# Performance work log

Hardware: AMD Instinct MI355X
Metric: run time of the kernel (lower is better)

The kernel has to match this reference:

```python
import jax, jax.numpy as jnp
import numpy as np

DT = 0.2   # dt
T = 30     # free-phase relaxation steps


def rho(x):
    return jnp.clip(x, 0.0, 1.0)


def rhop(x):
    return ((x >= 0.0) & (x <= 1.0)).astype(x.dtype)


def setup_inputs() -> dict:
    key = jax.random.key(0)
    ks = jax.random.split(key, 10)
    B = 2048
    L = [1024, 2048, 2048, 2048]  # fcLayers
    s0 = jax.random.uniform(ks[0], (B, L[0]), dtype=jnp.float32)
    s1 = jax.random.uniform(ks[1], (B, L[1]), dtype=jnp.float32)
    s2 = jax.random.uniform(ks[2], (B, L[2]), dtype=jnp.float32)
    data = jax.random.uniform(ks[3], (B, L[3]), dtype=jnp.float32)
    # W[i] = Linear(fcLayers[i+1], fcLayers[i]) -> weight [L[i], L[i+1]], fan_in = L[i+1]
    W0 = jax.random.normal(ks[4], (L[0], L[1]), dtype=jnp.float32) / np.float32(np.sqrt(L[1]))
    b0 = jax.random.normal(ks[5], (L[0],), dtype=jnp.float32) * np.float32(0.01)
    W1 = jax.random.normal(ks[6], (L[1], L[2]), dtype=jnp.float32) / np.float32(np.sqrt(L[2]))
    b1 = jax.random.normal(ks[7], (L[1],), dtype=jnp.float32) * np.float32(0.01)
    W2 = jax.random.normal(ks[8], (L[2], L[3]), dtype=jnp.float32) / np.float32(np.sqrt(L[3]))
    b2 = jax.random.normal(ks[9], (L[2],), dtype=jnp.float32) * np.float32(0.01)
    return {"s0": s0, "s1": s1, "s2": s2, "data": data,
            "W0": W0, "b0": b0, "W1": W1, "b1": b1, "W2": W2, "b2": b2}


def reference(s0, s1, s2, data, W0, b0, W1, b1, W2, b2):
    # Free-phase (beta=None, target=None, loss='MSE') -> stepper_c iterated T times.
    # s = [s0, s1, s2, data]; data (last element) is never updated.
    rd = rho(data)  # fixed input drive, precomputed once

    def step(carry, _):
        s0, s1, s2 = carry
        r0, r1, r2 = rho(s0), rho(s1), rho(s2)
        # dsdt[0] = -s0 + rhop(s0) * W0(rho(s1))
        d0 = -s0 + rhop(s0) * (r1 @ W0.T + b0)
        # dsdt[1] = -s1 + rhop(s1) * ( W1(rho(s2)) + rho(s0) @ W0 )
        d1 = -s1 + rhop(s1) * (r2 @ W1.T + b1 + r0 @ W0)
        # dsdt[2] = -s2 + rhop(s2) * ( W2(rho(data)) + rho(s1) @ W1 )
        d2 = -s2 + rhop(s2) * (rd @ W2.T + b2 + r1 @ W1)
        n0 = jnp.clip(s0 + DT * d0, 0.0, 1.0)
        n1 = jnp.clip(s1 + DT * d1, 0.0, 1.0)
        n2 = jnp.clip(s2 + DT * d2, 0.0, 1.0)
        return (n0, n1, n2), None

    (f0, f1, f2), _ = jax.lax.scan(step, (s0, s1, s2), None, length=T)
    return (f0, f1, f2)
```

## Files before the change

kernel.cpp:

```cpp
#include <hip/hip_runtime.h>
#include <stdint.h>

#define BM 128
#define BN 128
#define BK 64

typedef __bf16 bf16x8 __attribute__((ext_vector_type(8)));
typedef float f32x4 __attribute__((ext_vector_type(4)));

__device__ __forceinline__ float bf2f(uint16_t u) {
  union { uint32_t u32; float f; } x; x.u32 = ((uint32_t)u) << 16; return x.f;
}
__device__ __forceinline__ uint16_t f2bf(float f) {
  uint32_t x = __float_as_uint(f);
  uint32_t r = (x + 0x7FFFu + ((x >> 16) & 1u)) >> 16;
  return (uint16_t)r;
}

__device__ __forceinline__ void gload_lds16(const uint16_t* g, uint16_t* l) {
  __builtin_amdgcn_global_load_lds(
      (const __attribute__((address_space(1))) uint32_t*)g,
      (__attribute__((address_space(3))) uint32_t*)l, 16, 0, 0);
}

__device__ __forceinline__ void gemm_tile(
    const uint16_t* __restrict__ A, int ldA,
    const uint16_t* __restrict__ Bt, int ldB,
    int m0, int n0, int K,
    uint16_t* ldsA, uint16_t* ldsB, f32x4 acc[4][4])
{
  const int t  = threadIdx.x;
  const int ln = t & 63;
  const int wv = t >> 6;
  const int wr = wv >> 1, wc = wv & 1;

  const int row = t >> 3;
  const int gc  = (t & 7) ^ (row & 7);
  const uint16_t* ga = A  + (size_t)(m0 + row) * ldA + (gc << 3);
  const uint16_t* gb = Bt + (size_t)(n0 + row) * ldB + (gc << 3);
  uint16_t* la = ldsA + (t << 3);
  uint16_t* lb = ldsB + (t << 3);

  for (int kt = 0; kt < K; kt += BK) {
    __syncthreads();
#pragma unroll
    for (int c = 0; c < 4; ++c) {
      gload_lds16(ga + (size_t)(c * 32) * ldA, la + c * 2048);
      gload_lds16(gb + (size_t)(c * 32) * ldB, lb + c * 2048);
    }
    ga += BK; gb += BK;
    __syncthreads();

#pragma unroll
    for (int kk = 0; kk < 2; ++kk) {
      const int kc = (kk << 2) + (ln >> 4);
      const int sw = (kc ^ (ln & 7)) << 3;
      bf16x8 af[4], bfr[4];
#pragma unroll
      for (int mt = 0; mt < 4; ++mt)
        af[mt] = *(const bf16x8*)&ldsA[((wr << 6) + (mt << 4) + (ln & 15)) * BK + sw];
#pragma unroll
      for (int nt = 0; nt < 4; ++nt)
        bfr[nt] = *(const bf16x8*)&ldsB[((wc << 6) + (nt << 4) + (ln & 15)) * BK + sw];
#pragma unroll
      for (int mt = 0; mt < 4; ++mt)
#pragma unroll
        for (int nt = 0; nt < 4; ++nt)
          acc[mt][nt] = __builtin_amdgcn_mfma_f32_16x16x32_bf16(
              af[mt], bfr[nt], acc[mt][nt], 0, 0, 0);
    }
  }
}

__global__ void step_kernel(
    const uint16_t* __restrict__ s0b_c, const uint16_t* __restrict__ s1b_c,
    const uint16_t* __restrict__ s2b_c,
    uint16_t* __restrict__ s0b_n, uint16_t* __restrict__ s1b_n,
    uint16_t* __restrict__ s2b_n,
    const uint16_t* __restrict__ W0b, const uint16_t* __restrict__ W0Tb,
    const uint16_t* __restrict__ W1b, const uint16_t* __restrict__ W1Tb,
    const float* __restrict__ b0, const float* __restrict__ b1,
    const float* __restrict__ c2f,
    float* __restrict__ s0f, float* __restrict__ s1f, float* __restrict__ s2f)
{
  __shared__ uint16_t ldsA[BM * BK];
  __shared__ uint16_t ldsB[BN * BK];

  f32x4 acc[4][4];
  const f32x4 z = {0.f, 0.f, 0.f, 0.f};
#pragma unroll
  for (int i = 0; i < 4; ++i)
#pragma unroll
    for (int j = 0; j < 4; ++j) acc[i][j] = z;

  const int x = blockIdx.x & 7;
  const int j = blockIdx.x >> 3;
  const int c = j & 31;
  const int p = j >> 5;
  int mode, bm, bn;
  if (c < 16) {
    const int l = c + (p << 4);
    if (l < 16) { mode = 0; bm = (x << 1) + (l >> 3); bn = l & 7; }
    else { const int l2 = l - 16; mode = 2; bm = (x << 1) + (l2 >> 4); bn = l2 & 15; }
  } else {
    const int h = (c - 16) + (p << 4);
    mode = 1; bm = (x << 1) + (h >> 4); bn = h & 15;
  }

  if (mode == 0) {
    gemm_tile(s1b_c, 2048, W0b, 2048, bm * BM, bn * BN, 2048, ldsA, ldsB, acc);
  } else if (mode == 1) {
    gemm_tile(s2b_c, 2048, W1b, 2048, bm * BM, bn * BN, 2048, ldsA, ldsB, acc);
    gemm_tile(s0b_c, 1024, W0Tb, 1024, bm * BM, bn * BN, 1024, ldsA, ldsB, acc);
  } else {
    gemm_tile(s1b_c, 2048, W1Tb, 2048, bm * BM, bn * BN, 2048, ldsA, ldsB, acc);
  }

  const int t = threadIdx.x, wv = t >> 6, ln = t & 63;
  const int wr = wv >> 1, wc = wv & 1;
  const int rb = (ln >> 4) << 2, cc = ln & 15;
  const int m0 = bm * BM, n0 = bn * BN;

#pragma unroll
  for (int mt = 0; mt < 4; ++mt) {
#pragma unroll
    for (int nt = 0; nt < 4; ++nt) {
      const int gn = n0 + (wc << 6) + (nt << 4) + cc;
      float add = 0.f;
      if (mode == 0) add = b0[gn];
      else if (mode == 1) add = b1[gn];
#pragma unroll
      for (int r = 0; r < 4; ++r) {
        const int gm = m0 + (wr << 6) + (mt << 4) + rb + r;
        const float pre = acc[mt][nt][r];
        if (mode == 0) {
          const size_t ix = (size_t)gm * 1024 + gn;
          float nv = 0.8f * s0f[ix] + 0.2f * (pre + add);
          nv = fminf(fmaxf(nv, 0.f), 1.f);
          s0f[ix] = nv;
          s0b_n[ix] = f2bf(nv);
        } else if (mode == 1) {
          const size_t ix = (size_t)gm * 2048 + gn;
          float nv = 0.8f * s1f[ix] + 0.2f * (pre + add);
          nv = fminf(fmaxf(nv, 0.f), 1.f);
          s1f[ix] = nv;
          s1b_n[ix] = f2bf(nv);
        } else {
          const size_t ix = (size_t)gm * 2048 + gn;
          float nv = 0.8f * s2f[ix] + 0.2f * (pre + c2f[ix]);
          nv = fminf(fmaxf(nv, 0.f), 1.f);
          s2f[ix] = nv;
          s2b_n[ix] = f2bf(nv);
        }
      }
    }
  }
}

__global__ void c2_kernel(const uint16_t* __restrict__ datab,
                          const uint16_t* __restrict__ W2b,
                          const float* __restrict__ b2,
                          float* __restrict__ c2f)
{
  __shared__ uint16_t ldsA[BM * BK];
  __shared__ uint16_t ldsB[BN * BK];
  f32x4 acc[4][4];
  const f32x4 z = {0.f, 0.f, 0.f, 0.f};
#pragma unroll
  for (int i = 0; i < 4; ++i)
#pragma unroll
    for (int j = 0; j < 4; ++j) acc[i][j] = z;

  const int bm = blockIdx.x >> 4, bn = blockIdx.x & 15;
  gemm_tile(datab, 2048, W2b, 2048, bm * BM, bn * BN, 2048, ldsA, ldsB, acc);

  const int t = threadIdx.x, wv = t >> 6, ln = t & 63;
  const int wr = wv >> 1, wc = wv & 1;
  const int rb = (ln >> 4) << 2, cc = ln & 15;
  const int m0 = bm * BM, n0 = bn * BN;
#pragma unroll
  for (int mt = 0; mt < 4; ++mt)
#pragma unroll
    for (int nt = 0; nt < 4; ++nt) {
      const int gn = n0 + (wc << 6) + (nt << 4) + cc;
      const float bb = b2[gn];
#pragma unroll
      for (int r = 0; r < 4; ++r) {
        const int gm = m0 + (wr << 6) + (mt << 4) + rb + r;
        c2f[(size_t)gm * 2048 + gn] = acc[mt][nt][r] + bb;
      }
    }
}

__global__ void conv_k(const float* __restrict__ src, uint16_t* __restrict__ dst)
{
  const size_t i4 = ((size_t)blockIdx.x * 256 + threadIdx.x) << 2;
  const float4 v = *(const float4*)(src + i4);
  ushort4 o;
  o.x = f2bf(v.x); o.y = f2bf(v.y); o.z = f2bf(v.z); o.w = f2bf(v.w);
  *(ushort4*)(dst + i4) = o;
}

__global__ void convT_k(const float* __restrict__ src, uint16_t* __restrict__ dst,
                        int ldS, int ldD)
{
  __shared__ uint16_t tile[32][33];
  const int r0 = blockIdx.y * 32, c0 = blockIdx.x * 32;
  tile[threadIdx.y][threadIdx.x] =
      f2bf(src[(size_t)(r0 + threadIdx.y) * ldS + c0 + threadIdx.x]);
  __syncthreads();
  dst[(size_t)(c0 + threadIdx.y) * ldD + r0 + threadIdx.x] = tile[threadIdx.x][threadIdx.y];
}

__global__ void init_state(const float* __restrict__ in,
                           float* __restrict__ sf, uint16_t* __restrict__ sb)
{
  const size_t i4 = ((size_t)blockIdx.x * 256 + threadIdx.x) << 2;
  const float4 v = *(const float4*)(in + i4);
  *(float4*)(sf + i4) = v;
  ushort4 o;
  o.x = f2bf(v.x); o.y = f2bf(v.y); o.z = f2bf(v.z); o.w = f2bf(v.w);
  *(ushort4*)(sb + i4) = o;
}

extern "C" void kernel_launch(void* const* d_in, const int* in_sizes, int n_in,
                              void* d_out, int out_size, void* d_ws, size_t ws_size,
                              hipStream_t stream) {
  const float* s0   = (const float*)d_in[0];
  const float* s1   = (const float*)d_in[1];
  const float* s2   = (const float*)d_in[2];
  const float* data = (const float*)d_in[3];
  const float* W0   = (const float*)d_in[4];
  const float* b0   = (const float*)d_in[5];
  const float* W1   = (const float*)d_in[6];
  const float* b1   = (const float*)d_in[7];
  const float* W2   = (const float*)d_in[8];
  const float* b2   = (const float*)d_in[9];

  float* s0f = (float*)d_out;
  float* s1f = s0f + 2048ull * 1024;
  float* s2f = s1f + 2048ull * 2048;

  char* ws = (char*)d_ws;
  size_t off = 0;
  auto alloc = [&](size_t bytes) -> char* {
    char* p = ws + off; off += (bytes + 255) & ~(size_t)255; return p;
  };
  uint16_t* W0b    = (uint16_t*)alloc(1024ull * 2048 * 2);
  uint16_t* W0Tb   = (uint16_t*)alloc(2048ull * 1024 * 2);
  uint16_t* W1b    = (uint16_t*)alloc(2048ull * 2048 * 2);
  uint16_t* W1Tb   = (uint16_t*)alloc(2048ull * 2048 * 2);
  float*    c2f    = (float*)   alloc(2048ull * 2048 * 4);
  uint16_t* s0b[2] = { (uint16_t*)alloc(2048ull * 1024 * 2),
                       (uint16_t*)alloc(2048ull * 1024 * 2) };
  uint16_t* s1b[2] = { (uint16_t*)alloc(2048ull * 2048 * 2),
                       (uint16_t*)alloc(2048ull * 2048 * 2) };
  uint16_t* s2b[2] = { (uint16_t*)alloc(2048ull * 2048 * 2),
                       (uint16_t*)alloc(2048ull * 2048 * 2) };
  (void)ws_size; (void)in_sizes; (void)n_in; (void)out_size;

  conv_k<<<1024 * 2048 / 1024, 256, 0, stream>>>(W0, W0b);
  conv_k<<<2048 * 2048 / 1024, 256, 0, stream>>>(W1, W1b);
  dim3 tb(32, 32);
  convT_k<<<dim3(64, 32), tb, 0, stream>>>(W0, W0Tb, 2048, 1024);
  convT_k<<<dim3(64, 64), tb, 0, stream>>>(W1, W1Tb, 2048, 2048);
  conv_k<<<2048 * 2048 / 1024, 256, 0, stream>>>(data, s1b[1]);
  conv_k<<<2048 * 2048 / 1024, 256, 0, stream>>>(W2, s2b[1]);
  c2_kernel<<<256, 256, 0, stream>>>(s1b[1], s2b[1], b2, c2f);

  init_state<<<2048 * 1024 / 1024, 256, 0, stream>>>(s0, s0f, s0b[0]);
  init_state<<<2048 * 2048 / 1024, 256, 0, stream>>>(s1, s1f, s1b[0]);
  init_state<<<2048 * 2048 / 1024, 256, 0, stream>>>(s2, s2f, s2b[0]);

  for (int it = 0; it < 30; ++it) {
    const int c = it & 1, n = c ^ 1;
    step_kernel<<<640, 256, 0, stream>>>(
        s0b[c], s1b[c], s2b[c], s0b[n], s1b[n], s2b[n],
        W0b, W0Tb, W1b, W1Tb, b0, b1, c2f, s0f, s1f, s2f);
  }
}
```

Before: 2.423 ms.

## Schedule step tiles through per-group atomic work queues with heavy tiles first

The step kernel drops its fixed blockIdx-to-tile mapping over 640 blocks. It now launches 512 blocks that repeatedly claim tile indices from an atomic counter, one counter per row-group and per iteration. The costlier mode-1 tiles, which run two GEMMs, are handed out first, so the uneven per-tile work spreads across resident blocks instead of leaving a partial tail wave. This costs one atomic and one extra barrier per claimed tile, plus a small zeroing kernel for the counters.

```diff
diff --git a/kernel.cpp b/kernel.cpp
--- a/kernel.cpp
+++ b/kernel.cpp
@@ -81,76 +81,83 @@
     const uint16_t* __restrict__ W1b, const uint16_t* __restrict__ W1Tb,
     const float* __restrict__ b0, const float* __restrict__ b1,
     const float* __restrict__ c2f,
-    float* __restrict__ s0f, float* __restrict__ s1f, float* __restrict__ s2f)
+    float* __restrict__ s0f, float* __restrict__ s1f, float* __restrict__ s2f,
+    int* __restrict__ qcnt)
 {
   __shared__ uint16_t ldsA[BM * BK];
   __shared__ uint16_t ldsB[BN * BK];
-
-  f32x4 acc[4][4];
-  const f32x4 z = {0.f, 0.f, 0.f, 0.f};
-#pragma unroll
-  for (int i = 0; i < 4; ++i)
-#pragma unroll
-    for (int j = 0; j < 4; ++j) acc[i][j] = z;
+  __shared__ int sIdx;
 
   const int x = blockIdx.x & 7;
-  const int j = blockIdx.x >> 3;
-  const int c = j & 31;
-  const int p = j >> 5;
-  int mode, bm, bn;
-  if (c < 16) {
-    const int l = c + (p << 4);
-    if (l < 16) { mode = 0; bm = (x << 1) + (l >> 3); bn = l & 7; }
-    else { const int l2 = l - 16; mode = 2; bm = (x << 1) + (l2 >> 4); bn = l2 & 15; }
-  } else {
-    const int h = (c - 16) + (p << 4);
-    mode = 1; bm = (x << 1) + (h >> 4); bn = h & 15;
-  }
-
-  if (mode == 0) {
-    gemm_tile(s1b_c, 2048, W0b, 2048, bm * BM, bn * BN, 2048, ldsA, ldsB, acc);
-  } else if (mode == 1) {
-    gemm_tile(s2b_c, 2048, W1b, 2048, bm * BM, bn * BN, 2048, ldsA, ldsB, acc);
-    gemm_tile(s0b_c, 1024, W0Tb, 1024, bm * BM, bn * BN, 1024, ldsA, ldsB, acc);
-  } else {
-    gemm_tile(s1b_c, 2048, W1Tb, 2048, bm * BM, bn * BN, 2048, ldsA, ldsB, acc);
-  }
-
   const int t = threadIdx.x, wv = t >> 6, ln = t & 63;
   const int wr = wv >> 1, wc = wv & 1;
   const int rb = (ln >> 4) << 2, cc = ln & 15;
-  const int m0 = bm * BM, n0 = bn * BN;
-
-#pragma unroll
-  for (int mt = 0; mt < 4; ++mt) {
-#pragma unroll
-    for (int nt = 0; nt < 4; ++nt) {
-      const int gn = n0 + (wc << 6) + (nt << 4) + cc;
-      float add = 0.f;
-      if (mode == 0) add = b0[gn];
-      else if (mode == 1) add = b1[gn];
-#pragma unroll
-      for (int r = 0; r < 4; ++r) {
-        const int gm = m0 + (wr << 6) + (mt << 4) + rb + r;
-        const float pre = acc[mt][nt][r];
-        if (mode == 0) {
-          const size_t ix = (size_t)gm * 1024 + gn;
-          float nv = 0.8f * s0f[ix] + 0.2f * (pre + add);
-          nv = fminf(fmaxf(nv, 0.f), 1.f);
-          s0f[ix] = nv;
-          s0b_n[ix] = f2bf(nv);
-        } else if (mode == 1) {
-          const size_t ix = (size_t)gm * 2048 + gn;
-          float nv = 0.8f * s1f[ix] + 0.2f * (pre + add);
-          nv = fminf(fmaxf(nv, 0.f), 1.f);
-          s1f[ix] = nv;
-          s1b_n[ix] = f2bf(nv);
-        } else {
-          const size_t ix = (size_t)gm * 2048 + gn;
-          float nv = 0.8f * s2f[ix] + 0.2f * (pre + c2f[ix]);
-          nv = fminf(fmaxf(nv, 0.f), 1.f);
-          s2f[ix] = nv;
-          s2b_n[ix] = f2bf(nv);
+
+  for (;;) {
+    if (t == 0) sIdx = atomicAdd(&qcnt[x], 1);
+    __syncthreads();
+    const int idx = sIdx;
+    if (idx >= 80) break;
+
+    int mode, bm, bn;
+    if (idx < 32) {
+      mode = 1; bm = (x << 1) + (idx >> 4); bn = idx & 15;
+    } else if (idx < 48) {
+      const int l = idx - 32;
+      mode = 0; bm = (x << 1) + (l >> 3); bn = l & 7;
+    } else {
+      const int l = idx - 48;
+      mode = 2; bm = (x << 1) + (l >> 4); bn = l & 15;
+    }
+
+    f32x4 acc[4][4];
+    const f32x4 z = {0.f, 0.f, 0.f, 0.f};
+#pragma unroll
+    for (int i = 0; i < 4; ++i)
+#pragma unroll
+      for (int jj = 0; jj < 4; ++jj) acc[i][jj] = z;
+
+    if (mode == 0) {
+      gemm_tile(s1b_c, 2048, W0b, 2048, bm * BM, bn * BN, 2048, ldsA, ldsB, acc);
+    } else if (mode == 1) {
+      gemm_tile(s2b_c, 2048, W1b, 2048, bm * BM, bn * BN, 2048, ldsA, ldsB, acc);
+      gemm_tile(s0b_c, 1024, W0Tb, 1024, bm * BM, bn * BN, 1024, ldsA, ldsB, acc);
+    } else {
+      gemm_tile(s1b_c, 2048, W1Tb, 2048, bm * BM, bn * BN, 2048, ldsA, ldsB, acc);
+    }
+
+    const int m0 = bm * BM, n0 = bn * BN;
+#pragma unroll
+    for (int mt = 0; mt < 4; ++mt) {
+#pragma unroll
+      for (int nt = 0; nt < 4; ++nt) {
+        const int gn = n0 + (wc << 6) + (nt << 4) + cc;
+        float add = 0.f;
+        if (mode == 0) add = b0[gn];
+        else if (mode == 1) add = b1[gn];
+#pragma unroll
+        for (int r = 0; r < 4; ++r) {
+          const int gm = m0 + (wr << 6) + (mt << 4) + rb + r;
+          const float pre = acc[mt][nt][r];
+          if (mode == 0) {
+            const size_t ix = (size_t)gm * 1024 + gn;
+            float nv = 0.8f * s0f[ix] + 0.2f * (pre + add);
+            nv = fminf(fmaxf(nv, 0.f), 1.f);
+            s0f[ix] = nv;
+            s0b_n[ix] = f2bf(nv);
+          } else if (mode == 1) {
+            const size_t ix = (size_t)gm * 2048 + gn;
+            float nv = 0.8f * s1f[ix] + 0.2f * (pre + add);
+            nv = fminf(fmaxf(nv, 0.f), 1.f);
+            s1f[ix] = nv;
+            s1b_n[ix] = f2bf(nv);
+          } else {
+            const size_t ix = (size_t)gm * 2048 + gn;
+            float nv = 0.8f * s2f[ix] + 0.2f * (pre + c2f[ix]);
+            nv = fminf(fmaxf(nv, 0.f), 1.f);
+            s2f[ix] = nv;
+            s2b_n[ix] = f2bf(nv);
+          }
         }
       }
     }
@@ -222,6 +229,8 @@
   o.x = f2bf(v.x); o.y = f2bf(v.y); o.z = f2bf(v.z); o.w = f2bf(v.w);
   *(ushort4*)(sb + i4) = o;
 }
+
+__global__ void zeroq_k(int* __restrict__ q) { q[threadIdx.x] = 0; }
 
 extern "C" void kernel_launch(void* const* d_in, const int* in_sizes, int n_in,
                               void* d_out, int out_size, void* d_ws, size_t ws_size,
@@ -257,8 +266,10 @@
                        (uint16_t*)alloc(2048ull * 2048 * 2) };
   uint16_t* s2b[2] = { (uint16_t*)alloc(2048ull * 2048 * 2),
                        (uint16_t*)alloc(2048ull * 2048 * 2) };
+  int*      qcnt   = (int*)alloc(30 * 8 * sizeof(int));
   (void)ws_size; (void)in_sizes; (void)n_in; (void)out_size;
 
+  zeroq_k<<<1, 240, 0, stream>>>(qcnt);
   conv_k<<<1024 * 2048 / 1024, 256, 0, stream>>>(W0, W0b);
   conv_k<<<2048 * 2048 / 1024, 256, 0, stream>>>(W1, W1b);
   dim3 tb(32, 32);
@@ -274,8 +285,9 @@
 
   for (int it = 0; it < 30; ++it) {
     const int c = it & 1, n = c ^ 1;
-    step_kernel<<<640, 256, 0, stream>>>(
+    step_kernel<<<512, 256, 0, stream>>>(
         s0b[c], s1b[c], s2b[c], s0b[n], s1b[n], s2b[n],
-        W0b, W0Tb, W1b, W1Tb, b0, b1, c2f, s0f, s1f, s2f);
+        W0b, W0Tb, W1b, W1Tb, b0, b1, c2f, s0f, s1f, s2f,
+        qcnt + it * 8);
   }
 }
```

Result: slower. 3.765 ms (+55.4%).
